# Kernel optimization log

Measured on AMD Instinct MI355X. Metric: run time of the kernel, lower is better.

The kernel has to match this reference:

```python
import jax, jax.numpy as jnp
import numpy as np

N_DYADIC = 0   # init kwarg n: dyadic refinement order (0 = no refinement)


def _sig_kernel_gram(X, Y):
    """Signature-kernel Gram matrix via Goursat PDE solve (solver=0, linear kernel).

    X: (A, M, D), Y: (B, N, D). Returns K: (A, B) with K[a,b] = k_sig(x^a, y^b).
    PDE scheme: K[i+1,j+1] = K[i+1,j] + K[i,j+1] + K[i,j]*(inc[i,j] - 1),
    K[0,:] = K[:,0] = 1, inc[i,j] = <x_{i+1}-x_i, y_{j+1}-y_j>.
    The j-recursion is a prefix sum, so each row update is a vectorized cumsum;
    only the i-direction is sequential (lax.scan over M-1 rows).
    """
    dtype = X.dtype
    dX = X[:, 1:, :] - X[:, :-1, :]          # (A, M-1, D)
    dY = Y[:, 1:, :] - Y[:, :-1, :]          # (B, N-1, D)
    inc = jnp.einsum('amd,bnd->abmn', dX, dY)  # (A, B, M-1, N-1) increment grid
    if N_DYADIC > 0:
        f = 2 ** N_DYADIC
        inc = jnp.repeat(jnp.repeat(inc, f, axis=2), f, axis=3) / (f * f)
    A, B, M1, N1 = inc.shape
    ones_col = jnp.ones((A, B, 1), dtype)
    k0 = jnp.ones((A, B, N1 + 1), dtype)      # boundary row K[0, :] = 1

    def step(k_prev, inc_row):
        # k_new[j+1] = k_new[j] + (k_prev[j+1] - k_prev[j] + k_prev[j]*inc[j])
        delta = k_prev[..., 1:] - k_prev[..., :-1] + k_prev[..., :-1] * inc_row
        k_new = jnp.concatenate([ones_col, 1.0 + jnp.cumsum(delta, axis=-1)], axis=-1)
        return k_new, None

    k_last, _ = jax.lax.scan(step, k0, jnp.moveaxis(inc, 2, 0))
    return k_last[..., -1]                    # (A, B): K(s=T, t=T)


def setup_inputs() -> dict:
    key = jax.random.key(0)
    kx, ky = jax.random.split(key)
    # scale 0.1 keeps path increments moderate so the PDE solution stays well-conditioned
    X = jax.random.normal(kx, (64, 128, 64), dtype=jnp.float32) * 0.1
    Y = jax.random.normal(ky, (64, 128, 64), dtype=jnp.float32) * 0.1
    return {"X": X, "Y": Y}


def reference(X, Y):
    K_XX = _sig_kernel_gram(X, X)
    K_YY = _sig_kernel_gram(Y, Y)
    K_XY = _sig_kernel_gram(X, Y)
    dist = jnp.mean(K_XX) + jnp.mean(K_YY) - 2.0 * jnp.mean(K_XY)
    return jnp.mean((X[:, 0, :] - Y[:, 0, :]) ** 2) + dist
```

## Files before the change

kernel.cpp:

```cpp
#include <hip/hip_runtime.h>

#define AA   64
#define MM   128
#define DD   64
#define M1   127
#define CSTR 132
#define NXY  1024
#define NTRI 544
#define NBLK (NXY + 2*NTRI)
#define REG_I4 65536
#define PART_OFF (4u << 20)

typedef float f32x4 __attribute__((ext_vector_type(4)));
typedef short bf8_t __attribute__((ext_vector_type(8)));

template <int CTRL, int RM>
__device__ __forceinline__ float dpp0(float x) {
    return __int_as_float(
        __builtin_amdgcn_update_dpp(0, __float_as_int(x), CTRL, RM, 0xF, false));
}

__device__ __forceinline__ unsigned bf16_rne(float v) {
    unsigned u = __float_as_uint(v);
    return (u + 0x7FFFu + ((u >> 16) & 1u)) >> 16;
}
__device__ __forceinline__ float bf16_tof(unsigned h) {
    return __uint_as_float(h << 16);
}

__global__ __launch_bounds__(256) void prep_frags(const float* __restrict__ X,
                                                  const float* __restrict__ Y,
                                                  int4* __restrict__ frag) {
    const int tid = threadIdx.x, lane = tid & 63, w = tid >> 6;
    const int W    = blockIdx.x * 4 + w;
    const int inp  = W >> 9;
    const int p    = (W >> 3) & 63;
    const int tile = W & 7;
    const float* S = (inp ? Y : X) + p * (MM * DD);
    int i = tile * 16 + (lane & 15);
    if (i > 126) i = 126;
    const int d0 = (lane >> 4) << 3;

    int4* hi = frag + (inp * 2 + 0) * REG_I4;
    int4* lo = frag + (inp * 2 + 1) * REG_I4;
    const int base = p * 1024 + tile * 128 + lane;

    #pragma unroll
    for (int ks = 0; ks < 2; ++ks) {
        const float* r0 = S + i * DD + ks * 32 + d0;
        const float* r1 = r0 + DD;
        float4 a0 = *(const float4*)r0;
        float4 a1 = *(const float4*)(r0 + 4);
        float4 c0 = *(const float4*)r1;
        float4 c1 = *(const float4*)(r1 + 4);
        float v[8] = {c0.x - a0.x, c0.y - a0.y, c0.z - a0.z, c0.w - a0.w,
                      c1.x - a1.x, c1.y - a1.y, c1.z - a1.z, c1.w - a1.w};
        unsigned hs[8], ls[8];
        #pragma unroll
        for (int e = 0; e < 8; ++e) {
            hs[e] = bf16_rne(v[e]);
            ls[e] = bf16_rne(v[e] - bf16_tof(hs[e]));
        }
        int4 h, l;
        h.x = hs[0] | (hs[1] << 16); h.y = hs[2] | (hs[3] << 16);
        h.z = hs[4] | (hs[5] << 16); h.w = hs[6] | (hs[7] << 16);
        l.x = ls[0] | (ls[1] << 16); l.y = ls[2] | (ls[3] << 16);
        l.z = ls[4] | (ls[5] << 16); l.w = ls[6] | (ls[7] << 16);
        hi[base + ks * 64] = h;
        lo[base + ks * 64] = l;
    }
}

__global__ __launch_bounds__(256, 2)
void sig_pde(const int4* __restrict__ frag, float* __restrict__ partials) {
    const int tid = threadIdx.x, lane = tid & 63, w = tid >> 6;
    const int gid = blockIdx.x;

    int a, b, ain, bin;
    float wgt;
    if (gid < NXY) {
        b = gid >> 4; a = ((gid & 15) << 2) | w;
        ain = 0; bin = 1;
        wgt = -2.0f / 4096.0f;
    } else {
        int t = gid - NXY;
        int inp = 0;
        if (t >= NTRI) { t -= NTRI; inp = 1; }
        int q = (int)((__builtin_sqrtf((float)(2 * t + 1)) - 1.0f) * 0.5f);
        while (2 * (q + 1) * (q + 2) <= t) ++q;
        while (q > 0 && 2 * q * (q + 1) > t) --q;
        int r  = t - 2 * q * (q + 1);
        int i  = r / (q + 1);
        int ag = r - i * (q + 1);
        b = 4 * q + i; a = 4 * ag + w;
        ain = bin = inp;
        wgt = (a < b) ? (2.0f / 4096.0f) : ((a == b) ? (1.0f / 4096.0f) : 0.0f);
    }

    __shared__ int4  Bh[1024], Bl[1024];
    __shared__ float incS[4][16 * CSTR];
    __shared__ float red4[4];

    {
        const int4* Bhg = frag + (bin * 2 + 0) * REG_I4 + b * 1024;
        const int4* Blg = frag + (bin * 2 + 1) * REG_I4 + b * 1024;
        #pragma unroll
        for (int c = 0; c < 4; ++c) {
            int idx = c * 256 + tid;
            Bh[idx] = Bhg[idx];
            Bl[idx] = Blg[idx];
        }
    }
    __syncthreads();

    const int4* Ahg = frag + (ain * 2 + 0) * REG_I4 + a * 1024;
    const int4* Alg = frag + (ain * 2 + 1) * REG_I4 + a * 1024;

    int4 Ah[2], Al[2], Ahn[2], Aln[2];
    Ah[0] = Ahg[lane];      Ah[1] = Ahg[64 + lane];
    Al[0] = Alg[lane];      Al[1] = Alg[64 + lane];

    float k0 = 1.0f, k1 = 1.0f;
    float* incW = &incS[w][0];
    const int c2l = lane << 1;
    const int r0w = (lane >> 4) << 2, c0w = lane & 15;

    for (int strip = 0; strip < 8; ++strip) {
        if (strip < 7) {
            int off = (strip + 1) * 128 + lane;
            Ahn[0] = Ahg[off]; Ahn[1] = Ahg[off + 64];
            Aln[0] = Alg[off]; Aln[1] = Alg[off + 64];
        }

        f32x4 acc[8];
        #pragma unroll
        for (int t = 0; t < 8; ++t) acc[t] = (f32x4){0.f, 0.f, 0.f, 0.f};
        #pragma unroll
        for (int s = 0; s < 2; ++s) {
            bf8_t ah = __builtin_bit_cast(bf8_t, Ah[s]);
            bf8_t al = __builtin_bit_cast(bf8_t, Al[s]);
            #pragma unroll
            for (int t = 0; t < 8; ++t) {
                int fb = (t * 2 + s) * 64 + lane;
                bf8_t bh = *(const bf8_t*)&Bh[fb];
                bf8_t bl = *(const bf8_t*)&Bl[fb];
                acc[t] = __builtin_amdgcn_mfma_f32_16x16x32_bf16(ah, bh, acc[t], 0, 0, 0);
                acc[t] = __builtin_amdgcn_mfma_f32_16x16x32_bf16(ah, bl, acc[t], 0, 0, 0);
                acc[t] = __builtin_amdgcn_mfma_f32_16x16x32_bf16(al, bh, acc[t], 0, 0, 0);
            }
        }

        #pragma unroll
        for (int t = 0; t < 8; ++t) {
            float* pb = incW + r0w * CSTR + (t << 4) + c0w;
            pb[0]        = acc[t][0];
            pb[CSTR]     = acc[t][1];
            pb[2 * CSTR] = acc[t][2];
            pb[3 * CSTR] = acc[t][3];
        }

        const int rmax = (strip == 7) ? 15 : 16;
        for (int r = 0; r < rmax; ++r) {
            float2 sv = *(const float2*)(incW + r * CSTR + c2l);
            float s0 = sv.x, s1 = sv.y;
            float kp2 = dpp0<0x130, 0xF>(k0);
            float e0  = k1 - k0 + k0 * s0;
            float e1  = (lane < 63) ? (kp2 - k1 + k1 * s1) : 0.0f;
            float S = e0 + e1;
            S += dpp0<0x111, 0xF>(S);
            S += dpp0<0x112, 0xF>(S);
            S += dpp0<0x114, 0xF>(S);
            S += dpp0<0x118, 0xF>(S);
            S += dpp0<0x142, 0xA>(S);
            S += dpp0<0x143, 0xC>(S);
            float Sp = dpp0<0x138, 0xF>(S);
            k0 = 1.0f + Sp;
            k1 = 1.0f + S - e1;
        }

        Ah[0] = Ahn[0]; Ah[1] = Ahn[1];
        Al[0] = Aln[0]; Al[1] = Aln[1];
    }

    if (lane == 63) red4[w] = wgt * k1;
    __syncthreads();
    if (tid == 0)
        partials[gid] = red4[0] + red4[1] + red4[2] + red4[3];
}

__global__ void final_sum(const float* __restrict__ X, const float* __restrict__ Y,
                          const float* __restrict__ partials, float* __restrict__ out) {
    __shared__ float red[4];
    int tid = threadIdx.x;
    float acc = 0.f;
    for (int e = tid; e < NBLK; e += 256) acc += partials[e];
    for (int e = tid; e < AA * DD; e += 256) {
        int aa = e >> 6, d = e & 63;
        float df = X[aa * (MM * DD) + d] - Y[aa * (MM * DD) + d];
        acc = fmaf(df * df, 1.0f / 4096.0f, acc);
    }
    #pragma unroll
    for (int off = 32; off > 0; off >>= 1) acc += __shfl_down(acc, off);
    if ((tid & 63) == 0) red[tid >> 6] = acc;
    __syncthreads();
    if (tid == 0) out[0] = red[0] + red[1] + red[2] + red[3];
}

extern "C" void kernel_launch(void* const* d_in, const int* in_sizes, int n_in,
                              void* d_out, int out_size, void* d_ws, size_t ws_size,
                              hipStream_t stream) {
    const float* X = (const float*)d_in[0];
    const float* Y = (const float*)d_in[1];
    float* out = (float*)d_out;
    int4*  frag = (int4*)d_ws;
    float* partials = (float*)((char*)d_ws + PART_OFF);

    hipLaunchKernelGGL(prep_frags, dim3(256), dim3(256), 0, stream, X, Y, frag);
    hipLaunchKernelGGL(sig_pde, dim3(NBLK), dim3(256), 0, stream, frag, partials);
    hipLaunchKernelGGL(final_sum, dim3(1), dim3(256), 0, stream, X, Y, partials, out);
}
```

Baseline: 160.9 us.

## Fuse final reduction into PDE kernel and hand-code DPP scan in inline asm

The separate final_sum launch is removed; each PDE block publishes its partial with a release store and bumps an atomic counter, and the last block to finish does the global reduction. The counter is zeroed in prep_frags. The per-row scan now uses inline-asm DPP adds with s_nop padding, FMA-fused row updates, and a 16-row register preload of the increment strip from LDS. This saves one kernel launch and some LDS latency in the serial loop, at the cost of atomics, fragile inline asm and higher register pressure.

```diff
diff --git a/kernel.cpp b/kernel.cpp
--- a/kernel.cpp
+++ b/kernel.cpp
@@ -14,12 +14,6 @@
 typedef float f32x4 __attribute__((ext_vector_type(4)));
 typedef short bf8_t __attribute__((ext_vector_type(8)));
 
-template <int CTRL, int RM>
-__device__ __forceinline__ float dpp0(float x) {
-    return __int_as_float(
-        __builtin_amdgcn_update_dpp(0, __float_as_int(x), CTRL, RM, 0xF, false));
-}
-
 __device__ __forceinline__ unsigned bf16_rne(float v) {
     unsigned u = __float_as_uint(v);
     return (u + 0x7FFFu + ((u >> 16) & 1u)) >> 16;
@@ -30,8 +24,10 @@
 
 __global__ __launch_bounds__(256) void prep_frags(const float* __restrict__ X,
                                                   const float* __restrict__ Y,
-                                                  int4* __restrict__ frag) {
+                                                  int4* __restrict__ frag,
+                                                  unsigned* __restrict__ ctr) {
     const int tid = threadIdx.x, lane = tid & 63, w = tid >> 6;
+    if (blockIdx.x == 0 && tid == 0) *ctr = 0u;
     const int W    = blockIdx.x * 4 + w;
     const int inp  = W >> 9;
     const int p    = (W >> 3) & 63;
@@ -72,7 +68,10 @@
 }
 
 __global__ __launch_bounds__(256, 2)
-void sig_pde(const int4* __restrict__ frag, float* __restrict__ partials) {
+void sig_pde(const int4* __restrict__ frag, float* __restrict__ partials,
+             unsigned* __restrict__ ctr,
+             const float* __restrict__ X, const float* __restrict__ Y,
+             float* __restrict__ out) {
     const int tid = threadIdx.x, lane = tid & 63, w = tid >> 6;
     const int gid = blockIdx.x;
 
@@ -100,6 +99,7 @@
     __shared__ int4  Bh[1024], Bl[1024];
     __shared__ float incS[4][16 * CSTR];
     __shared__ float red4[4];
+    __shared__ int   amLast;
 
     {
         const int4* Bhg = frag + (bin * 2 + 0) * REG_I4 + b * 1024;
@@ -159,23 +159,40 @@
             pb[3 * CSTR] = acc[t][3];
         }
 
+        float2 rowv[16];
+        #pragma unroll
+        for (int r = 0; r < 16; ++r)
+            rowv[r] = *(const float2*)(incW + r * CSTR + c2l);
+
         const int rmax = (strip == 7) ? 15 : 16;
         for (int r = 0; r < rmax; ++r) {
-            float2 sv = *(const float2*)(incW + r * CSTR + c2l);
-            float s0 = sv.x, s1 = sv.y;
-            float kp2 = dpp0<0x130, 0xF>(k0);
-            float e0  = k1 - k0 + k0 * s0;
-            float e1  = (lane < 63) ? (kp2 - k1 + k1 * s1) : 0.0f;
+            float s0 = rowv[r].x, s1 = rowv[r].y;
+            float kp2;
+            asm("s_nop 1\n\t"
+                "v_mov_b32_dpp %0, %1 wave_shl:1 row_mask:0xf bank_mask:0xf bound_ctrl:0"
+                : "=v"(kp2) : "v"(k0));
+            float e0 = __builtin_fmaf(k0, s0, k1 - k0);
+            float e1 = __builtin_fmaf(k1, s1, kp2 - k1);
+            e1 = (lane < 63) ? e1 : 0.0f;
             float S = e0 + e1;
-            S += dpp0<0x111, 0xF>(S);
-            S += dpp0<0x112, 0xF>(S);
-            S += dpp0<0x114, 0xF>(S);
-            S += dpp0<0x118, 0xF>(S);
-            S += dpp0<0x142, 0xA>(S);
-            S += dpp0<0x143, 0xC>(S);
-            float Sp = dpp0<0x138, 0xF>(S);
+            asm("s_nop 1\n\t"
+                "v_add_f32_dpp %0, %0, %0 row_shr:1 row_mask:0xf bank_mask:0xf bound_ctrl:0" : "+v"(S));
+            asm("s_nop 1\n\t"
+                "v_add_f32_dpp %0, %0, %0 row_shr:2 row_mask:0xf bank_mask:0xf bound_ctrl:0" : "+v"(S));
+            asm("s_nop 1\n\t"
+                "v_add_f32_dpp %0, %0, %0 row_shr:4 row_mask:0xf bank_mask:0xf bound_ctrl:0" : "+v"(S));
+            asm("s_nop 1\n\t"
+                "v_add_f32_dpp %0, %0, %0 row_shr:8 row_mask:0xf bank_mask:0xf bound_ctrl:0" : "+v"(S));
+            asm("s_nop 1\n\t"
+                "v_add_f32_dpp %0, %0, %0 row_bcast:15 row_mask:0xa bank_mask:0xf bound_ctrl:0" : "+v"(S));
+            asm("s_nop 1\n\t"
+                "v_add_f32_dpp %0, %0, %0 row_bcast:31 row_mask:0xc bank_mask:0xf bound_ctrl:0" : "+v"(S));
+            float Sp;
+            asm("s_nop 1\n\t"
+                "v_mov_b32_dpp %0, %1 wave_shr:1 row_mask:0xf bank_mask:0xf bound_ctrl:0"
+                : "=v"(Sp) : "v"(S));
             k0 = 1.0f + Sp;
-            k1 = 1.0f + S - e1;
+            k1 = 1.0f + (S - e1);
         }
 
         Ah[0] = Ahn[0]; Ah[1] = Ahn[1];
@@ -184,26 +201,32 @@
 
     if (lane == 63) red4[w] = wgt * k1;
     __syncthreads();
-    if (tid == 0)
-        partials[gid] = red4[0] + red4[1] + red4[2] + red4[3];
-}
-
-__global__ void final_sum(const float* __restrict__ X, const float* __restrict__ Y,
-                          const float* __restrict__ partials, float* __restrict__ out) {
-    __shared__ float red[4];
-    int tid = threadIdx.x;
-    float acc = 0.f;
-    for (int e = tid; e < NBLK; e += 256) acc += partials[e];
-    for (int e = tid; e < AA * DD; e += 256) {
-        int aa = e >> 6, d = e & 63;
-        float df = X[aa * (MM * DD) + d] - Y[aa * (MM * DD) + d];
-        acc = fmaf(df * df, 1.0f / 4096.0f, acc);
-    }
-    #pragma unroll
-    for (int off = 32; off > 0; off >>= 1) acc += __shfl_down(acc, off);
-    if ((tid & 63) == 0) red[tid >> 6] = acc;
+    if (tid == 0) {
+        float s = red4[0] + red4[1] + red4[2] + red4[3];
+        __hip_atomic_store(&partials[gid], s, __ATOMIC_RELEASE,
+                           __HIP_MEMORY_SCOPE_AGENT);
+        unsigned prev = __hip_atomic_fetch_add(ctr, 1u, __ATOMIC_ACQ_REL,
+                                               __HIP_MEMORY_SCOPE_AGENT);
+        amLast = (prev == NBLK - 1);
+    }
     __syncthreads();
-    if (tid == 0) out[0] = red[0] + red[1] + red[2] + red[3];
+    if (amLast) {
+        float acc = 0.f;
+        for (int e = tid; e < NBLK; e += 256)
+            acc += __hip_atomic_load(&partials[e], __ATOMIC_ACQUIRE,
+                                     __HIP_MEMORY_SCOPE_AGENT);
+        for (int e = tid; e < AA * DD; e += 256) {
+            int aa = e >> 6, d = e & 63;
+            float df = X[aa * (MM * DD) + d] - Y[aa * (MM * DD) + d];
+            acc = __builtin_fmaf(df * df, 1.0f / 4096.0f, acc);
+        }
+        #pragma unroll
+        for (int off = 32; off > 0; off >>= 1) acc += __shfl_down(acc, off);
+        __syncthreads();
+        if ((tid & 63) == 0) red4[tid >> 6] = acc;
+        __syncthreads();
+        if (tid == 0) out[0] = red4[0] + red4[1] + red4[2] + red4[3];
+    }
 }
 
 extern "C" void kernel_launch(void* const* d_in, const int* in_sizes, int n_in,
@@ -214,8 +237,9 @@
     float* out = (float*)d_out;
     int4*  frag = (int4*)d_ws;
     float* partials = (float*)((char*)d_ws + PART_OFF);
-
-    hipLaunchKernelGGL(prep_frags, dim3(256), dim3(256), 0, stream, X, Y, frag);
-    hipLaunchKernelGGL(sig_pde, dim3(NBLK), dim3(256), 0, stream, frag, partials);
-    hipLaunchKernelGGL(final_sum, dim3(1), dim3(256), 0, stream, X, Y, partials, out);
-}
+    unsigned* ctr = (unsigned*)((char*)d_ws + PART_OFF + NBLK * sizeof(float));
+
+    hipLaunchKernelGGL(prep_frags, dim3(256), dim3(256), 0, stream, X, Y, frag, ctr);
+    hipLaunchKernelGGL(sig_pde, dim3(NBLK), dim3(256), 0, stream,
+                       frag, partials, ctr, X, Y, out);
+}
```

New measurement: 374.0 us. +132.4%, slower.
